# Performance work log

Measured on AMD Instinct MI355X. Metric: run time of the kernel, lower is better.

## Reference

```python
import jax, jax.numpy as jnp
import numpy as np

D_MODEL = 1024
D_HEAD = 64
M_BITS = 32


def setup_inputs() -> dict:
    key = jax.random.key(0)
    ks = jax.random.split(key, 6)
    B, N, M = 2, 2048, 2048
    Q = jax.random.normal(ks[0], (B, N, D_MODEL), dtype=jnp.float32)
    K = jax.random.normal(ks[1], (B, M, D_MODEL), dtype=jnp.float32)
    V = jax.random.normal(ks[2], (B, M, D_MODEL), dtype=jnp.float32)
    s = 1.0 / np.sqrt(D_MODEL)
    Wq = jax.random.normal(ks[3], (D_MODEL, M_BITS), dtype=jnp.float32) * s
    Wk = jax.random.normal(ks[4], (D_MODEL, M_BITS), dtype=jnp.float32) * s
    Wv = jax.random.normal(ks[5], (D_MODEL, D_HEAD), dtype=jnp.float32) * s
    temperature = jnp.ones((1,), dtype=jnp.float32)
    return {"Q": Q, "K": K, "V": V, "Wq": Wq, "Wk": Wk, "Wv": Wv,
            "temperature": temperature}


def tropical_matmul(A, Bt):
    # A: [B, N, m], Bt: [B, M, m] (already transposed form of [B, m, M])
    # (A \odot B)_{ij} = min_k (A_ik + B_kj)
    return jnp.min(A[:, :, None, :] + Bt[:, None, :, :], axis=-1)  # [B, N, M]


def reference(Q, K, V, Wq, Wk, Wv, temperature):
    # REWA tropical encoders (continuous): linear projections to m_bits
    Qt = jnp.einsum('bnd,dm->bnm', Q, Wq)   # [B, N, m_bits]
    Kt = jnp.einsum('bsd,dm->bsm', K, Wk)   # [B, M, m_bits]
    Vp = jnp.einsum('bsd,dh->bsh', V, Wv)   # [B, M, d_head]
    # tropical (min-plus) scores, negated so shorter paths score higher
    scores = -tropical_matmul(Qt, Kt)       # [B, N, M]
    scores = scores / jax.nn.softplus(temperature[0])
    attn = jax.nn.softmax(scores, axis=-1)  # [B, N, M]
    out = jnp.einsum('bnm,bmh->bnh', attn, Vp)  # [B, N, d_head]
    return out, attn
```

## Files before the change

kernel.cpp:

```cpp
#include <hip/hip_runtime.h>
#include <math.h>

#define DM 1024
#define NB 2048
#define MBITS 32
#define DH 64

typedef __attribute__((ext_vector_type(4))) float floatx4;
typedef __attribute__((ext_vector_type(8))) short shortx8;

__device__ __forceinline__ unsigned short f32_to_bf16(float f) {
    union { float f; unsigned u; } v; v.f = f;
    unsigned r = v.u + 0x7FFF + ((v.u >> 16) & 1);
    return (unsigned short)(r >> 16);
}

__global__ __launch_bounds__(256) void trop_proj_kernel(
    const float* __restrict__ Q, const float* __restrict__ K, const float* __restrict__ V,
    const float* __restrict__ Wq, const float* __restrict__ Wk, const float* __restrict__ Wv,
    float* __restrict__ Qt, float* __restrict__ Kt, float* __restrict__ Vp)
{
    __shared__ float Xs[64][68];
    __shared__ float Ws[32][68];

    int bx = blockIdx.x, kq = blockIdx.y;
    const float* X; const float* W; int C, c0, job, rb;
    if (bx < 64)       { job = 0; rb = bx;        X = Q; W = Wq; C = 32; c0 = 0; }
    else if (bx < 128) { job = 1; rb = bx - 64;   X = K; W = Wk; C = 32; c0 = 0; }
    else { job = 2; int z = bx - 128; rb = z >> 1; X = V; W = Wv; C = 64; c0 = (z & 1) * 32; }
    int r0 = rb * 64;
    int t  = threadIdx.x;
    int rg = t >> 3;
    int cg = t & 7;

    float acc[2][4] = {{0,0,0,0},{0,0,0,0}};

    for (int kc = kq * 4; kc < kq * 4 + 4; ++kc) {
        __syncthreads();
        #pragma unroll
        for (int u = 0; u < 4; ++u) {
            int flat4 = u * 256 + t;
            int row = flat4 >> 4, c4 = flat4 & 15;
            floatx4 g = *(const floatx4*)&X[(size_t)(r0 + row) * DM + kc * 64 + c4 * 4];
            *(floatx4*)&Xs[row][c4 * 4] = g;
        }
        #pragma unroll
        for (int u = 0; u < 2; ++u) {
            int flat4 = u * 256 + t;
            int k = flat4 >> 3, c4 = flat4 & 7;
            floatx4 g = *(const floatx4*)&W[(size_t)(kc * 64 + k) * C + c0 + c4 * 4];
            Ws[c4 * 4 + 0][k] = g.x;
            Ws[c4 * 4 + 1][k] = g.y;
            Ws[c4 * 4 + 2][k] = g.z;
            Ws[c4 * 4 + 3][k] = g.w;
        }
        __syncthreads();
        #pragma unroll
        for (int k4 = 0; k4 < 16; ++k4) {
            floatx4 x0 = *(const floatx4*)&Xs[2 * rg + 0][k4 * 4];
            floatx4 x1 = *(const floatx4*)&Xs[2 * rg + 1][k4 * 4];
            #pragma unroll
            for (int ci = 0; ci < 4; ++ci) {
                floatx4 w4 = *(const floatx4*)&Ws[cg + 8 * ci][k4 * 4];
                acc[0][ci] += x0.x * w4.x + x0.y * w4.y + x0.z * w4.z + x0.w * w4.w;
                acc[1][ci] += x1.x * w4.x + x1.y * w4.y + x1.z * w4.z + x1.w * w4.w;
            }
        }
    }

    float* Y = (job == 0) ? Qt : (job == 1) ? Kt : Vp;
    int Cout = (job == 2) ? 64 : 32;
    #pragma unroll
    for (int ri = 0; ri < 2; ++ri)
        #pragma unroll
        for (int ci = 0; ci < 4; ++ci)
            atomicAdd(&Y[(size_t)(r0 + 2 * rg + ri) * Cout + c0 + cg + 8 * ci], acc[ri][ci]);
}

__global__ __launch_bounds__(256) void vp_transpose_kernel(
    const float* __restrict__ Vp, unsigned short* __restrict__ VpT)
{
    __shared__ float Ls[32][68];
    int r0 = blockIdx.x * 32;
    int t  = threadIdx.x;
    #pragma unroll
    for (int u = 0; u < 2; ++u) {
        int flat4 = u * 256 + t;
        int row = flat4 >> 4, c4 = flat4 & 15;
        *(floatx4*)&Ls[row][c4 * 4] = *(const floatx4*)&Vp[(size_t)(r0 + row) * DH + c4 * 4];
    }
    __syncthreads();
    int b = r0 >> 11, j0 = r0 & 2047;
    #pragma unroll
    for (int u = 0; u < 8; ++u) {
        int flat = u * 256 + t;
        int h = flat >> 5, j = flat & 31;
        VpT[(size_t)b * (DH * NB) + (size_t)h * NB + j0 + j] = f32_to_bf16(Ls[j][h]);
    }
}

__global__ __launch_bounds__(256) void trop_score_kernel(
    const float* __restrict__ Qt, const float* __restrict__ Kt,
    const float* __restrict__ temp, float* __restrict__ partial,
    float* __restrict__ attn)
{
    __shared__ float Qs[16][36];
    __shared__ float Ks[256][36];

    int b  = blockIdx.z;
    int jc = blockIdx.y;
    int i0 = blockIdx.x * 16;
    int t  = threadIdx.x;
    int w  = t >> 6, l = t & 63;

    if (t < 128) {
        int row = t >> 3, k4 = t & 7;
        *(floatx4*)&Qs[row][k4 * 4] =
            *(const floatx4*)&Qt[(size_t)(b * NB + i0 + row) * MBITS + k4 * 4];
    }
    #pragma unroll
    for (int u = 0; u < 8; ++u) {
        int flat4 = u * 256 + t;
        int row = flat4 >> 3, k4 = flat4 & 7;
        *(floatx4*)&Ks[row][k4 * 4] =
            *(const floatx4*)&Kt[(size_t)(b * NB + jc * 256 + row) * MBITS + k4 * 4];
    }
    float tv = temp[0];
    float c2 = -(1.0f / log1pf(__expf(tv))) * 1.44269504088896340736f;
    __syncthreads();

    float m[4][4];
    #pragma unroll
    for (int ii = 0; ii < 4; ++ii)
        #pragma unroll
        for (int jj = 0; jj < 4; ++jj) m[ii][jj] = 1e30f;

    #pragma unroll
    for (int k4 = 0; k4 < 8; ++k4) {
        floatx4 q[4], kk[4];
        #pragma unroll
        for (int ii = 0; ii < 4; ++ii) q[ii] = *(const floatx4*)&Qs[w + 4 * ii][k4 * 4];
        #pragma unroll
        for (int jj = 0; jj < 4; ++jj) kk[jj] = *(const floatx4*)&Ks[l + 64 * jj][k4 * 4];
        #pragma unroll
        for (int ii = 0; ii < 4; ++ii)
            #pragma unroll
            for (int jj = 0; jj < 4; ++jj) {
                float a0 = q[ii].x + kk[jj].x;
                float a1 = q[ii].y + kk[jj].y;
                float a2 = q[ii].z + kk[jj].z;
                float a3 = q[ii].w + kk[jj].w;
                m[ii][jj] = fminf(m[ii][jj], fminf(fminf(a0, a1), fminf(a2, a3)));
            }
    }

    float psum[4];
    #pragma unroll
    for (int ii = 0; ii < 4; ++ii) {
        int i = w + 4 * ii;
        float s = 0.f;
        #pragma unroll
        for (int jj = 0; jj < 4; ++jj) {
            int j = l + 64 * jj;
            float e = exp2f(c2 * m[ii][jj]);
            attn[(size_t)(b * NB + i0 + i) * 2048 + jc * 256 + j] = e;
            s += e;
        }
        psum[ii] = s;
    }

    #pragma unroll
    for (int ii = 0; ii < 4; ++ii) {
        float v = psum[ii];
        #pragma unroll
        for (int off = 1; off < 64; off <<= 1) v += __shfl_xor(v, off, 64);
        if (l == 0) partial[((size_t)b * NB + i0 + w + 4 * ii) * 8 + jc] = v;
    }
}

__global__ __launch_bounds__(256) void trop_out_kernel(
    const unsigned short* __restrict__ VpT, const float* __restrict__ partial,
    float* __restrict__ outp, float* __restrict__ attn)
{
    __shared__ unsigned short Vs[64][256];
    __shared__ unsigned short Es[16][264];
    __shared__ float inv_s[16];

    int b  = blockIdx.z;
    int jc = blockIdx.y;
    int i0 = blockIdx.x * 16;
    int t  = threadIdx.x;
    int w  = t >> 6, l = t & 63;

    #pragma unroll
    for (int u = 0; u < 8; ++u) {
        int flat16 = u * 256 + t;
        int h = flat16 >> 5, c = flat16 & 31;
        uint4 g = *(const uint4*)&VpT[(size_t)b * (DH * NB) + (size_t)h * NB + jc * 256 + c * 8];
        *(uint4*)&Vs[h][(c ^ (h & 31)) * 8] = g;
    }
    if (t < 16) {
        float s = 0.f;
        #pragma unroll
        for (int p = 0; p < 8; ++p) s += partial[((size_t)b * NB + i0 + t) * 8 + p];
        inv_s[t] = 1.0f / s;
    }
    __syncthreads();

    #pragma unroll
    for (int u = 0; u < 4; ++u) {
        int flat4 = u * 256 + t;
        int row = flat4 >> 6, c4 = flat4 & 63;
        size_t g = (size_t)(b * NB + i0 + row) * 2048 + jc * 256 + c4 * 4;
        floatx4 e4 = *(const floatx4*)&attn[g];
        float iv = inv_s[row];
        e4.x *= iv; e4.y *= iv; e4.z *= iv; e4.w *= iv;
        *(floatx4*)&attn[g] = e4;
        unsigned u0 = (unsigned)f32_to_bf16(e4.x) | ((unsigned)f32_to_bf16(e4.y) << 16);
        unsigned u1 = (unsigned)f32_to_bf16(e4.z) | ((unsigned)f32_to_bf16(e4.w) << 16);
        uint2 pk; pk.x = u0; pk.y = u1;
        *(uint2*)&Es[row][c4 * 4] = pk;
    }
    __syncthreads();

    floatx4 acc = {0.f, 0.f, 0.f, 0.f};
    #pragma unroll
    for (int kk = 0; kk < 8; ++kk) {
        int mrow = l & 15, q4 = l >> 4;
        shortx8 a = *(const shortx8*)&Es[mrow][kk * 32 + q4 * 8];
        int h = w * 16 + mrow;
        int c = kk * 4 + q4;
        shortx8 bf = *(const shortx8*)&Vs[h][(c ^ (h & 31)) * 8];
        acc = __builtin_amdgcn_mfma_f32_16x16x32_bf16(a, bf, acc, 0, 0, 0);
    }

    #pragma unroll
    for (int r = 0; r < 4; ++r) {
        int irow = (l >> 4) * 4 + r;
        atomicAdd(&outp[(size_t)(b * NB + i0 + irow) * DH + w * 16 + (l & 15)], acc[r]);
    }
}

extern "C" void kernel_launch(void* const* d_in, const int* in_sizes, int n_in,
                              void* d_out, int out_size, void* d_ws, size_t ws_size,
                              hipStream_t stream) {
    (void)in_sizes; (void)n_in; (void)out_size; (void)ws_size;
    const float* Q    = (const float*)d_in[0];
    const float* K    = (const float*)d_in[1];
    const float* V    = (const float*)d_in[2];
    const float* Wq   = (const float*)d_in[3];
    const float* Wk   = (const float*)d_in[4];
    const float* Wv   = (const float*)d_in[5];
    const float* temp = (const float*)d_in[6];

    float* outp = (float*)d_out;
    float* attn = outp + 2 * 2048 * 64;

    float* wsf = (float*)d_ws;
    float* Qt      = wsf;
    float* Kt      = wsf + 131072;
    float* Vp      = wsf + 262144;
    float* partial = wsf + 524288;
    unsigned short* VpT = (unsigned short*)(wsf + 557056);

    hipMemsetAsync(d_ws, 0, 524288 * sizeof(float), stream);
    hipMemsetAsync(d_out, 0, 262144 * sizeof(float), stream);

    trop_proj_kernel<<<dim3(256, 4), 256, 0, stream>>>(Q, K, V, Wq, Wk, Wv, Qt, Kt, Vp);
    vp_transpose_kernel<<<128, 256, 0, stream>>>(Vp, VpT);
    trop_score_kernel<<<dim3(128, 8, 2), 256, 0, stream>>>(Qt, Kt, temp, partial, attn);
    trop_out_kernel<<<dim3(128, 8, 2), 256, 0, stream>>>(VpT, partial, outp, attn);
}
```

Baseline: 164.7 us.

## Use split-bf16 MFMA projections and a bf16 intermediate exp buffer

Replaces the scalar fp32 projection kernel with an MFMA projection. Inputs and pre-split weights are each split into hi/lo bf16 parts and combined with three MFMAs. Each tile now writes its full result directly, so the atomics, the workspace memset and the separate Vp transpose kernel go away; V projections are written straight into the bf16 transposed layout. When the workspace is large enough, the score kernel stores unnormalized exponentials as bf16 in scratch instead of fp32 in the attn output. The output kernel then reads them back, normalizes them into attn, and applies 1/sum after the MFMA, which cuts global memory traffic on the largest tensor. The cost is extra bf16 rounding of the attn values and a dependence on the workspace size.

After: 182.6 us. 10.9% more time.

```diff
diff --git a/kernel.cpp b/kernel.cpp
--- a/kernel.cpp
+++ b/kernel.cpp
@@ -15,94 +15,130 @@
     return (unsigned short)(r >> 16);
 }
 
-__global__ __launch_bounds__(256) void trop_proj_kernel(
+__device__ __forceinline__ void split2(float x0, float x1, unsigned& hp, unsigned& lp) {
+    union { float f; unsigned u; } a, b; a.f = x0; b.f = x1;
+    unsigned h0 = a.u & 0xFFFF0000u, h1 = b.u & 0xFFFF0000u;
+    union { unsigned u; float f; } hf0, hf1; hf0.u = h0; hf1.u = h1;
+    union { float f; unsigned u; } c, d;
+    c.f = x0 - hf0.f;
+    d.f = x1 - hf1.f;
+    hp = (h0 >> 16) | h1;
+    lp = (c.u >> 16) | (d.u & 0xFFFF0000u);
+}
+
+__global__ __launch_bounds__(256) void wprep_kernel(
+    const float* __restrict__ Wq, const float* __restrict__ Wk,
+    const float* __restrict__ Wv, unsigned short* __restrict__ Wf)
+{
+    int wv = blockIdx.x * 4 + (threadIdx.x >> 6);
+    int l  = threadIdx.x & 63;
+    const float* W; int C, kc32, ct;
+    if (wv < 64)       { W = Wq; C = 32; kc32 = wv >> 1;  ct = wv & 1; }
+    else if (wv < 128) { W = Wk; C = 32; int z = wv - 64;  kc32 = z >> 1; ct = z & 1; }
+    else               { W = Wv; C = 64; int z = wv - 128; kc32 = z >> 2; ct = z & 3; }
+    int k0 = kc32 * 32 + (l >> 4) * 8;
+    int c  = ct * 16 + (l & 15);
+    float x[8];
+    #pragma unroll
+    for (int j = 0; j < 8; ++j) x[j] = W[(size_t)(k0 + j) * C + c];
+    unsigned hp[4], lp[4];
+    #pragma unroll
+    for (int j2 = 0; j2 < 4; ++j2) split2(x[2 * j2], x[2 * j2 + 1], hp[j2], lp[j2]);
+    uint4 hv; hv.x = hp[0]; hv.y = hp[1]; hv.z = hp[2]; hv.w = hp[3];
+    uint4 lv; lv.x = lp[0]; lv.y = lp[1]; lv.z = lp[2]; lv.w = lp[3];
+    *(uint4*)&Wf[(size_t)wv * 1024 + l * 8]       = hv;
+    *(uint4*)&Wf[(size_t)wv * 1024 + 512 + l * 8] = lv;
+}
+
+__global__ __launch_bounds__(64) void proj_mfma_kernel(
     const float* __restrict__ Q, const float* __restrict__ K, const float* __restrict__ V,
-    const float* __restrict__ Wq, const float* __restrict__ Wk, const float* __restrict__ Wv,
-    float* __restrict__ Qt, float* __restrict__ Kt, float* __restrict__ Vp)
+    const unsigned short* __restrict__ Wf,
+    float* __restrict__ Qt, float* __restrict__ Kt, unsigned short* __restrict__ VpT)
 {
-    __shared__ float Xs[64][68];
-    __shared__ float Ws[32][68];
-
-    int bx = blockIdx.x, kq = blockIdx.y;
-    const float* X; const float* W; int C, c0, job, rb;
-    if (bx < 64)       { job = 0; rb = bx;        X = Q; W = Wq; C = 32; c0 = 0; }
-    else if (bx < 128) { job = 1; rb = bx - 64;   X = K; W = Wk; C = 32; c0 = 0; }
-    else { job = 2; int z = bx - 128; rb = z >> 1; X = V; W = Wv; C = 64; c0 = (z & 1) * 32; }
-    int r0 = rb * 64;
-    int t  = threadIdx.x;
-    int rg = t >> 3;
-    int cg = t & 7;
-
-    float acc[2][4] = {{0,0,0,0},{0,0,0,0}};
-
-    for (int kc = kq * 4; kc < kq * 4 + 4; ++kc) {
+    __shared__ unsigned short Xhi[16][72];
+    __shared__ unsigned short Xlo[16][72];
+
+    int gb = blockIdx.x;
+    int job = gb >> 8, tile = gb & 255;
+    int r0 = tile * 16;
+    const float* X = (job == 0) ? Q : (job == 1) ? K : V;
+    int ntct  = (job == 2) ? 4 : 2;
+    int pbase = job << 6;
+    int l = threadIdx.x;
+    int lrow = l & 15, lq = l >> 4;
+
+    floatx4 acc[4];
+    #pragma unroll
+    for (int i = 0; i < 4; ++i) acc[i] = (floatx4){0.f, 0.f, 0.f, 0.f};
+
+    floatx4 g[4];
+    #pragma unroll
+    for (int q = 0; q < 4; ++q)
+        g[q] = *(const floatx4*)&X[(size_t)(r0 + q * 4 + lq) * DM + lrow * 4];
+
+    for (int c = 0; c < 16; ++c) {
+        floatx4 gn[4];
+        if (c < 15) {
+            #pragma unroll
+            for (int q = 0; q < 4; ++q)
+                gn[q] = *(const floatx4*)&X[(size_t)(r0 + q * 4 + lq) * DM + (c + 1) * 64 + lrow * 4];
+        }
         __syncthreads();
         #pragma unroll
-        for (int u = 0; u < 4; ++u) {
-            int flat4 = u * 256 + t;
-            int row = flat4 >> 4, c4 = flat4 & 15;
-            floatx4 g = *(const floatx4*)&X[(size_t)(r0 + row) * DM + kc * 64 + c4 * 4];
-            *(floatx4*)&Xs[row][c4 * 4] = g;
-        }
-        #pragma unroll
-        for (int u = 0; u < 2; ++u) {
-            int flat4 = u * 256 + t;
-            int k = flat4 >> 3, c4 = flat4 & 7;
-            floatx4 g = *(const floatx4*)&W[(size_t)(kc * 64 + k) * C + c0 + c4 * 4];
-            Ws[c4 * 4 + 0][k] = g.x;
-            Ws[c4 * 4 + 1][k] = g.y;
-            Ws[c4 * 4 + 2][k] = g.z;
-            Ws[c4 * 4 + 3][k] = g.w;
+        for (int q = 0; q < 4; ++q) {
+            unsigned h01, l01, h23, l23;
+            split2(g[q].x, g[q].y, h01, l01);
+            split2(g[q].z, g[q].w, h23, l23);
+            uint2 hh; hh.x = h01; hh.y = h23;
+            uint2 ll; ll.x = l01; ll.y = l23;
+            *(uint2*)&Xhi[q * 4 + lq][lrow * 4] = hh;
+            *(uint2*)&Xlo[q * 4 + lq][lrow * 4] = ll;
         }
         __syncthreads();
         #pragma unroll
-        for (int k4 = 0; k4 < 16; ++k4) {
-            floatx4 x0 = *(const floatx4*)&Xs[2 * rg + 0][k4 * 4];
-            floatx4 x1 = *(const floatx4*)&Xs[2 * rg + 1][k4 * 4];
-            #pragma unroll
-            for (int ci = 0; ci < 4; ++ci) {
-                floatx4 w4 = *(const floatx4*)&Ws[cg + 8 * ci][k4 * 4];
-                acc[0][ci] += x0.x * w4.x + x0.y * w4.y + x0.z * w4.z + x0.w * w4.w;
-                acc[1][ci] += x1.x * w4.x + x1.y * w4.y + x1.z * w4.z + x1.w * w4.w;
+        for (int sub = 0; sub < 2; ++sub) {
+            shortx8 ahi = *(const shortx8*)&Xhi[lrow][sub * 32 + lq * 8];
+            shortx8 alo = *(const shortx8*)&Xlo[lrow][sub * 32 + lq * 8];
+            int kc32 = c * 2 + sub;
+            for (int ct = 0; ct < ntct; ++ct) {
+                int p = pbase + kc32 * ntct + ct;
+                const unsigned short* wp = &Wf[(size_t)p * 1024 + l * 8];
+                shortx8 bhi = *(const shortx8*)wp;
+                shortx8 blo = *(const shortx8*)(wp + 512);
+                acc[ct] = __builtin_amdgcn_mfma_f32_16x16x32_bf16(ahi, bhi, acc[ct], 0, 0, 0);
+                acc[ct] = __builtin_amdgcn_mfma_f32_16x16x32_bf16(ahi, blo, acc[ct], 0, 0, 0);
+                acc[ct] = __builtin_amdgcn_mfma_f32_16x16x32_bf16(alo, bhi, acc[ct], 0, 0, 0);
             }
         }
-    }
-
-    float* Y = (job == 0) ? Qt : (job == 1) ? Kt : Vp;
-    int Cout = (job == 2) ? 64 : 32;
-    #pragma unroll
-    for (int ri = 0; ri < 2; ++ri)
-        #pragma unroll
-        for (int ci = 0; ci < 4; ++ci)
-            atomicAdd(&Y[(size_t)(r0 + 2 * rg + ri) * Cout + c0 + cg + 8 * ci], acc[ri][ci]);
-}
-
-__global__ __launch_bounds__(256) void vp_transpose_kernel(
-    const float* __restrict__ Vp, unsigned short* __restrict__ VpT)
-{
-    __shared__ float Ls[32][68];
-    int r0 = blockIdx.x * 32;
-    int t  = threadIdx.x;
-    #pragma unroll
-    for (int u = 0; u < 2; ++u) {
-        int flat4 = u * 256 + t;
-        int row = flat4 >> 4, c4 = flat4 & 15;
-        *(floatx4*)&Ls[row][c4 * 4] = *(const floatx4*)&Vp[(size_t)(r0 + row) * DH + c4 * 4];
-    }
-    __syncthreads();
-    int b = r0 >> 11, j0 = r0 & 2047;
-    #pragma unroll
-    for (int u = 0; u < 8; ++u) {
-        int flat = u * 256 + t;
-        int h = flat >> 5, j = flat & 31;
-        VpT[(size_t)b * (DH * NB) + (size_t)h * NB + j0 + j] = f32_to_bf16(Ls[j][h]);
-    }
-}
-
+        #pragma unroll
+        for (int q = 0; q < 4; ++q) g[q] = gn[q];
+    }
+
+    if (job < 2) {
+        float* Y = (job == 0) ? Qt : Kt;
+        #pragma unroll
+        for (int ct = 0; ct < 2; ++ct)
+            #pragma unroll
+            for (int r = 0; r < 4; ++r)
+                Y[(size_t)(r0 + lq * 4 + r) * MBITS + ct * 16 + lrow] = acc[ct][r];
+    } else {
+        #pragma unroll
+        for (int ct = 0; ct < 4; ++ct)
+            #pragma unroll
+            for (int r = 0; r < 4; ++r) {
+                int row = r0 + lq * 4 + r;
+                int b = row >> 11, j = row & 2047;
+                VpT[(size_t)b * (DH * NB) + (size_t)(ct * 16 + lrow) * NB + j] =
+                    f32_to_bf16(acc[ct][r]);
+            }
+    }
+}
+
+template <typename ET>
 __global__ __launch_bounds__(256) void trop_score_kernel(
     const float* __restrict__ Qt, const float* __restrict__ Kt,
     const float* __restrict__ temp, float* __restrict__ partial,
-    float* __restrict__ attn)
+    ET* __restrict__ ebuf)
 {
     __shared__ float Qs[16][36];
     __shared__ float Ks[256][36];
@@ -150,7 +186,7 @@
                 float a1 = q[ii].y + kk[jj].y;
                 float a2 = q[ii].z + kk[jj].z;
                 float a3 = q[ii].w + kk[jj].w;
-                m[ii][jj] = fminf(m[ii][jj], fminf(fminf(a0, a1), fminf(a2, a3)));
+                m[ii][jj] = fminf(fminf(m[ii][jj], fminf(a0, a1)), fminf(a2, a3));
             }
     }
 
@@ -163,7 +199,9 @@
         for (int jj = 0; jj < 4; ++jj) {
             int j = l + 64 * jj;
             float e = exp2f(c2 * m[ii][jj]);
-            attn[(size_t)(b * NB + i0 + i) * 2048 + jc * 256 + j] = e;
+            size_t idx = (size_t)(b * NB + i0 + i) * 2048 + jc * 256 + j;
+            if (sizeof(ET) == 2) ebuf[idx] = (ET)f32_to_bf16(e);
+            else                 ebuf[idx] = (ET)e;
             s += e;
         }
         psum[ii] = s;
@@ -178,9 +216,10 @@
     }
 }
 
+template <bool EBF16>
 __global__ __launch_bounds__(256) void trop_out_kernel(
     const unsigned short* __restrict__ VpT, const float* __restrict__ partial,
-    float* __restrict__ outp, float* __restrict__ attn)
+    const void* __restrict__ ebuf_in, float* __restrict__ outp, float* __restrict__ attn)
 {
     __shared__ unsigned short Vs[64][256];
     __shared__ unsigned short Es[16][264];
@@ -205,21 +244,52 @@
         for (int p = 0; p < 8; ++p) s += partial[((size_t)b * NB + i0 + t) * 8 + p];
         inv_s[t] = 1.0f / s;
     }
-    __syncthreads();
-
-    #pragma unroll
-    for (int u = 0; u < 4; ++u) {
-        int flat4 = u * 256 + t;
-        int row = flat4 >> 6, c4 = flat4 & 63;
-        size_t g = (size_t)(b * NB + i0 + row) * 2048 + jc * 256 + c4 * 4;
-        floatx4 e4 = *(const floatx4*)&attn[g];
+
+    if (EBF16) {
+        const unsigned short* eb = (const unsigned short*)ebuf_in;
+        #pragma unroll
+        for (int u = 0; u < 2; ++u) {
+            int flat = u * 256 + t;
+            int row = flat >> 5, c = flat & 31;
+            uint4 g = *(const uint4*)&eb[(size_t)(b * NB + i0 + row) * 2048 + jc * 256 + c * 8];
+            *(uint4*)&Es[row][c * 8] = g;
+        }
+        __syncthreads();
+        int row = t >> 4, cb = (t & 15) * 16;
         float iv = inv_s[row];
-        e4.x *= iv; e4.y *= iv; e4.z *= iv; e4.w *= iv;
-        *(floatx4*)&attn[g] = e4;
-        unsigned u0 = (unsigned)f32_to_bf16(e4.x) | ((unsigned)f32_to_bf16(e4.y) << 16);
-        unsigned u1 = (unsigned)f32_to_bf16(e4.z) | ((unsigned)f32_to_bf16(e4.w) << 16);
-        uint2 pk; pk.x = u0; pk.y = u1;
-        *(uint2*)&Es[row][c4 * 4] = pk;
+        #pragma unroll
+        for (int h8 = 0; h8 < 2; ++h8) {
+            uint4 e8 = *(const uint4*)&Es[row][cb + h8 * 8];
+            unsigned uu[4] = {e8.x, e8.y, e8.z, e8.w};
+            float f[8];
+            #pragma unroll
+            for (int z = 0; z < 4; ++z) {
+                union { unsigned u; float f; } v0, v1;
+                v0.u = uu[z] << 16; v1.u = uu[z] & 0xFFFF0000u;
+                f[2 * z] = v0.f * iv; f[2 * z + 1] = v1.f * iv;
+            }
+            size_t gidx = (size_t)(b * NB + i0 + row) * 2048 + jc * 256 + cb + h8 * 8;
+            floatx4 o0; o0.x = f[0]; o0.y = f[1]; o0.z = f[2]; o0.w = f[3];
+            floatx4 o1; o1.x = f[4]; o1.y = f[5]; o1.z = f[6]; o1.w = f[7];
+            *(floatx4*)&attn[gidx]     = o0;
+            *(floatx4*)&attn[gidx + 4] = o1;
+        }
+    } else {
+        __syncthreads();
+        #pragma unroll
+        for (int u = 0; u < 4; ++u) {
+            int flat4 = u * 256 + t;
+            int row = flat4 >> 6, c4 = flat4 & 63;
+            size_t g = (size_t)(b * NB + i0 + row) * 2048 + jc * 256 + c4 * 4;
+            floatx4 e4 = *(const floatx4*)&attn[g];
+            float iv = inv_s[row];
+            unsigned u0 = (unsigned)f32_to_bf16(e4.x) | ((unsigned)f32_to_bf16(e4.y) << 16);
+            unsigned u1 = (unsigned)f32_to_bf16(e4.z) | ((unsigned)f32_to_bf16(e4.w) << 16);
+            uint2 pk; pk.x = u0; pk.y = u1;
+            *(uint2*)&Es[row][c4 * 4] = pk;
+            e4.x *= iv; e4.y *= iv; e4.z *= iv; e4.w *= iv;
+            *(floatx4*)&attn[g] = e4;
+        }
     }
     __syncthreads();
 
@@ -237,14 +307,15 @@
     #pragma unroll
     for (int r = 0; r < 4; ++r) {
         int irow = (l >> 4) * 4 + r;
-        atomicAdd(&outp[(size_t)(b * NB + i0 + irow) * DH + w * 16 + (l & 15)], acc[r]);
+        atomicAdd(&outp[(size_t)(b * NB + i0 + irow) * DH + w * 16 + (l & 15)],
+                  acc[r] * inv_s[irow]);
     }
 }
 
 extern "C" void kernel_launch(void* const* d_in, const int* in_sizes, int n_in,
                               void* d_out, int out_size, void* d_ws, size_t ws_size,
                               hipStream_t stream) {
-    (void)in_sizes; (void)n_in; (void)out_size; (void)ws_size;
+    (void)in_sizes; (void)n_in; (void)out_size;
     const float* Q    = (const float*)d_in[0];
     const float* K    = (const float*)d_in[1];
     const float* V    = (const float*)d_in[2];
@@ -256,18 +327,29 @@
     float* outp = (float*)d_out;
     float* attn = outp + 2 * 2048 * 64;
 
-    float* wsf = (float*)d_ws;
-    float* Qt      = wsf;
-    float* Kt      = wsf + 131072;
-    float* Vp      = wsf + 262144;
-    float* partial = wsf + 524288;
-    unsigned short* VpT = (unsigned short*)(wsf + 557056);
-
-    hipMemsetAsync(d_ws, 0, 524288 * sizeof(float), stream);
+    char* ws = (char*)d_ws;
+    float*          Qt      = (float*)(ws);
+    float*          Kt      = (float*)(ws + 524288);
+    float*          partial = (float*)(ws + 1048576);
+    unsigned short* Wf      = (unsigned short*)(ws + 1179648);
+    unsigned short* VpT     = (unsigned short*)(ws + 1703936);
+    unsigned short* Ebuf    = (unsigned short*)(ws + 2228224);
+    bool bf16path = ws_size >= (size_t)2228224 + 33554432;
+
     hipMemsetAsync(d_out, 0, 262144 * sizeof(float), stream);
 
-    trop_proj_kernel<<<dim3(256, 4), 256, 0, stream>>>(Q, K, V, Wq, Wk, Wv, Qt, Kt, Vp);
-    vp_transpose_kernel<<<128, 256, 0, stream>>>(Vp, VpT);
-    trop_score_kernel<<<dim3(128, 8, 2), 256, 0, stream>>>(Qt, Kt, temp, partial, attn);
-    trop_out_kernel<<<dim3(128, 8, 2), 256, 0, stream>>>(VpT, partial, outp, attn);
-}
+    wprep_kernel<<<64, 256, 0, stream>>>(Wq, Wk, Wv, Wf);
+    proj_mfma_kernel<<<768, 64, 0, stream>>>(Q, K, V, Wf, Qt, Kt, VpT);
+
+    if (bf16path) {
+        trop_score_kernel<unsigned short><<<dim3(128, 8, 2), 256, 0, stream>>>(
+            Qt, Kt, temp, partial, Ebuf);
+        trop_out_kernel<true><<<dim3(128, 8, 2), 256, 0, stream>>>(
+            VpT, partial, Ebuf, outp, attn);
+    } else {
+        trop_score_kernel<float><<<dim3(128, 8, 2), 256, 0, stream>>>(
+            Qt, Kt, temp, partial, attn);
+        trop_out_kernel<false><<<dim3(128, 8, 2), 256, 0, stream>>>(
+            VpT, partial, attn, outp, attn);
+    }
+}
```
